# Optimization experiments

Measured on AMD Instinct MI355X. Metric: run time of the kernel, lower is better.

## Reference

```python
import jax, jax.numpy as jnp
import numpy as np

B, L, CIN, C = 256, 65, 2053, 512
SCALE = 1.0 / float(np.sqrt(C))


def _attn_layer(x, Wq, bq, Wk, bk, Wv, bv):
    # x: [B, Cin, L]; Conv1d(kernel=1) == channel-mixing matmul
    q = jnp.einsum('oi,bil->bol', Wq, x) + bq[:, None]
    k = jnp.einsum('oi,bil->bol', Wk, x) + bk[:, None]
    v = jax.nn.leaky_relu(jnp.einsum('oi,bil->bol', Wv, x) + bv[:, None], 0.01)
    # att[b,l,m] = <q[:,l], k[:,m]> / sqrt(C); softmax over m
    att = jax.nn.softmax(jnp.einsum('bcl,bcm->blm', q, k) * SCALE, axis=-1)
    # original: sum_m att[b,l,1,m] * v[b,1,c,m] -> [B,L,C] -> permute -> [B,C,L]
    out = jnp.einsum('blm,bcm->bcl', att, v)
    return out + x if out.shape == x.shape else out  # residual only when channels match


def _transform(x, Wq0, bq0, Wk0, bk0, Wv0, bv0, Wq, bq, Wk, bk, Wv, bv):
    x = _attn_layer(x, Wq0, bq0, Wk0, bk0, Wv0, bv0)
    for n in range(3):  # layers 1..3, C->C with residual
        x = _attn_layer(x, Wq[n], bq[n], Wk[n], bk[n], Wv[n], bv[n])
    return x


def setup_inputs():
    key = jax.random.key(0)
    ks = jax.random.split(key, 20)
    s = 0.02
    inp = {
        'dataleft': jax.random.normal(ks[0], (B, L, CIN), jnp.float32),
        'dataright': jax.random.normal(ks[1], (B, L, CIN), jnp.float32),
        # layer-0 QKV conv1d (k=1) weights: [C, CIN]
        'Wq0': jax.random.normal(ks[2], (C, CIN), jnp.float32) * s,
        'bq0': jnp.zeros((C,), jnp.float32),
        'Wk0': jax.random.normal(ks[3], (C, CIN), jnp.float32) * s,
        'bk0': jnp.zeros((C,), jnp.float32),
        'Wv0': jax.random.normal(ks[4], (C, CIN), jnp.float32) * s,
        'bv0': jnp.zeros((C,), jnp.float32),
        # layers 1..3 stacked: [3, C, C]
        'Wq': jax.random.normal(ks[5], (3, C, C), jnp.float32) * s,
        'bq': jnp.zeros((3, C), jnp.float32),
        'Wk': jax.random.normal(ks[6], (3, C, C), jnp.float32) * s,
        'bk': jnp.zeros((3, C), jnp.float32),
        'Wv': jax.random.normal(ks[7], (3, C, C), jnp.float32) * s,
        'bv': jnp.zeros((3, C), jnp.float32),
        # classifier: fc1(1024->256), fc2(256->2)
        'W1': jax.random.normal(ks[8], (256, 2 * C), jnp.float32) * s,
        'b1': jnp.zeros((256,), jnp.float32),
        'W2': jax.random.normal(ks[9], (2, 256), jnp.float32) * s,
        'b2': jnp.zeros((2,), jnp.float32),
    }
    return inp


def reference(dataleft, dataright, Wq0, bq0, Wk0, bk0, Wv0, bv0,
              Wq, bq, Wk, bk, Wv, bv, W1, b1, W2, b2):
    xl = jnp.transpose(dataleft, (0, 2, 1))   # [B, CIN, L]
    xr = jnp.transpose(dataright, (0, 2, 1))
    xl = _transform(xl, Wq0, bq0, Wk0, bk0, Wv0, bv0, Wq, bq, Wk, bk, Wv, bv)
    xr = _transform(xr, Wq0, bq0, Wk0, bk0, Wv0, bv0, Wq, bq, Wk, bk, Wv, bv)
    # AdaptiveAvgPool2d((512,1)) on [B,512,L]: identity over channel dim, mean over L
    xl = jnp.mean(xl, axis=-1)  # [B, C]
    xr = jnp.mean(xr, axis=-1)
    h = jnp.concatenate([xl, xr], axis=1)            # [B, 2C]
    h = jax.nn.relu(h @ W1.T + b1)                   # [B, 256]
    y = h @ W2.T + b2                                # [B, 2]
    return y  # training mode: no final softmax
```

## Files before the change

### kernel.cpp

```cpp
#include <hip/hip_runtime.h>
#include <hip/hip_bf16.h>

#define BF16 __hip_bfloat16

typedef __bf16 bf16x8 __attribute__((ext_vector_type(8)));
typedef float f32x4 __attribute__((ext_vector_type(4)));

__device__ __forceinline__ void async_copy16(const void* g, void* l) {
    __builtin_amdgcn_global_load_lds(
        (const __attribute__((address_space(1))) void*)g,
        (__attribute__((address_space(3))) void*)l,
        16, 0, 0);
}

__global__ __launch_bounds__(256) void convert_pad_k(
    const float* __restrict__ src, BF16* __restrict__ dst,
    int Ks, int Kd) {
    const long r = blockIdx.y;
    const int k = (blockIdx.x * 256 + threadIdx.x) * 4;
    if (k >= Kd) return;
    const float* s = src + r * (long)Ks;
    float a0 = (k < Ks) ? s[k] : 0.f;
    float a1 = (k + 1 < Ks) ? s[k + 1] : 0.f;
    float a2 = (k + 2 < Ks) ? s[k + 2] : 0.f;
    float a3 = (k + 3 < Ks) ? s[k + 3] : 0.f;
    BF16 b0 = __float2bfloat16(a0), b1 = __float2bfloat16(a1);
    BF16 b2 = __float2bfloat16(a2), b3 = __float2bfloat16(a3);
    ushort4 o = make_ushort4(*(ushort*)&b0, *(ushort*)&b1, *(ushort*)&b2, *(ushort*)&b3);
    *(ushort4*)&dst[r * (long)Kd + k] = o;
}

template <int K>
__device__ __forceinline__ void gemm_body(
    const BF16* __restrict__ Xg, const BF16* __restrict__ Wg,
    const float* __restrict__ bqp, const float* __restrict__ bkp, const float* __restrict__ bvp,
    BF16* __restrict__ Qo, BF16* __restrict__ Ko, BF16* __restrict__ Vo) {
    __shared__ __align__(16) BF16 As[3][256 * 32];
    __shared__ __align__(16) BF16 Bs[3][128 * 32];
    const int tid = threadIdx.x;
    const int w = tid >> 6;
    const int lane = tid & 63;
    const int quad = lane >> 4;
    const int l15 = lane & 15;
    const int linear = blockIdx.x + 12 * blockIdx.y;
    const int cpx = (12 * (int)gridDim.y) >> 3;
    const int id2 = (linear & 7) * cpx + (linear >> 3);
    const int bx = id2 % 12;
    const int by = id2 / 12;
    const long n0 = (long)by * 256;
    const long m0full = (long)bx * 128;
    const int sel = bx >> 2;
    const int mbase = (bx & 3) * 128;
    const int wr = (w >> 1) * 64;
    const int wc = (w & 1) * 64;
    constexpr int KT = K >> 5;
    const int rw = w * 16 + (lane >> 2);
    const int gsw = ((lane & 3) ^ ((lane >> 3) & 3)) * 8;
    const int gx = (quad ^ ((l15 >> 1) & 3)) * 8;

#define STAGE_TILE(k0, buf)                                                              \
    do {                                                                                 \
        _Pragma("unroll")                                                                \
        for (int r_ = 0; r_ < 2; ++r_)                                                   \
            async_copy16(Xg + (n0 + r_ * 128 + rw) * K + (k0) + gsw,                     \
                         &As[buf][(r_ * 128 + w * 16) * 32]);                            \
        async_copy16(Wg + (m0full + rw) * K + (k0) + gsw,                                \
                     &Bs[buf][(w * 16) * 32]);                                           \
    } while (0)

    f32x4 acc[4][4] = {};
    STAGE_TILE(0, 0);
    STAGE_TILE(32, 1);
    int cb = 0;
    for (int kt = 0; kt < KT; ++kt) {
        if (kt + 1 < KT) {
            asm volatile("s_waitcnt vmcnt(3)\n\ts_barrier" ::: "memory");
        } else {
            asm volatile("s_waitcnt vmcnt(0)\n\ts_barrier" ::: "memory");
        }
        __builtin_amdgcn_sched_barrier(0);
        bf16x8 af[4], bfr[4];
#pragma unroll
        for (int i = 0; i < 4; ++i)
            af[i] = *(const bf16x8*)&As[cb][(wr + i * 16 + l15) * 32 + gx];
#pragma unroll
        for (int j = 0; j < 4; ++j)
            bfr[j] = *(const bf16x8*)&Bs[cb][(wc + j * 16 + l15) * 32 + gx];
        if (kt + 2 < KT) {
            int nb = cb + 2;
            if (nb >= 3) nb -= 3;
            STAGE_TILE((kt + 2) << 5, nb);
        }
        __builtin_amdgcn_s_setprio(1);
#pragma unroll
        for (int i = 0; i < 4; ++i)
#pragma unroll
            for (int j = 0; j < 4; ++j)
                acc[i][j] = __builtin_amdgcn_mfma_f32_16x16x32_bf16(af[i], bfr[j], acc[i][j], 0, 0, 0);
        __builtin_amdgcn_s_setprio(0);
        ++cb;
        if (cb >= 3) cb -= 3;
    }
#undef STAGE_TILE

    const float* bp = (sel == 0) ? bqp : (sel == 1) ? bkp : bvp;
    BF16* out = (sel == 0) ? Qo : (sel == 1) ? Ko : Vo;
#pragma unroll
    for (int j = 0; j < 4; ++j) {
        const int m = mbase + wc + j * 16 + l15;
        const float bz = bp[m];
#pragma unroll
        for (int i = 0; i < 4; ++i) {
#pragma unroll
            for (int r = 0; r < 4; ++r) {
                const long n = n0 + wr + i * 16 + quad * 4 + r;
                float v = acc[i][j][r] + bz;
                if (sel == 2) v = (v >= 0.f) ? v : 0.01f * v;
                out[n * 512 + m] = __float2bfloat16(v);
            }
        }
    }
}

__global__ __launch_bounds__(512, 2) void gemm_k2112(
    const BF16* __restrict__ Xg, const BF16* __restrict__ Wg,
    const float* __restrict__ bqp, const float* __restrict__ bkp, const float* __restrict__ bvp,
    BF16* __restrict__ Qo, BF16* __restrict__ Ko, BF16* __restrict__ Vo) {
    gemm_body<2112>(Xg, Wg, bqp, bkp, bvp, Qo, Ko, Vo);
}

__global__ __launch_bounds__(512, 2) void gemm_k512(
    const BF16* __restrict__ Xg, const BF16* __restrict__ Wg,
    const float* __restrict__ bqp, const float* __restrict__ bkp, const float* __restrict__ bvp,
    BF16* __restrict__ Qo, BF16* __restrict__ Ko, BF16* __restrict__ Vo) {
    gemm_body<512>(Xg, Wg, bqp, bkp, bvp, Qo, Ko, Vo);
}

__global__ __launch_bounds__(256) void attn_fused(
    const BF16* __restrict__ Qg, const BF16* __restrict__ Kg, const BF16* __restrict__ Vg,
    BF16* __restrict__ Xg, int residual) {
    constexpr float SC = 0.04419417382415922f;
    __shared__ __align__(16) char Us[26624];
    __shared__ float Sf[80 * 84];
    __shared__ __align__(16) BF16 Pl[80 * 104];
    BF16* qk = (BF16*)Us;
    BF16* Vtl = (BF16*)Us;
    const int bb = blockIdx.x;
    const int tid = threadIdx.x;
    const int w = tid >> 6, lane = tid & 63, quad = lane >> 4, l15 = lane & 15;

    int i16a[7], j16a[7];
#pragma unroll
    for (int u = 0; u < 7; ++u) {
        const int t = w + 4 * u;
        const int tc = (t < 25) ? t : 0;
        i16a[u] = (tc / 5) * 16;
        j16a[u] = (tc % 5) * 16;
    }
    f32x4 acc[7] = {};
    for (int k0 = 0; k0 < 512; k0 += 64) {
        for (int idx = tid; idx < 1280; idx += 256) {
            const int t = (idx >= 640) ? 1 : 0;
            const int e = idx - t * 640;
            const int sub = (e >= 320) ? 1 : 0;
            const int e2 = e - sub * 320;
            const int row = e2 >> 2;
            const int koff = (e2 & 3) * 8;
            uint4 val = make_uint4(0, 0, 0, 0);
            if (row < 65) {
                const BF16* src = (t ? Kg : Qg) + ((long)(bb * 65 + row) * 512 + k0 + sub * 32 + koff);
                val = *(const uint4*)src;
            }
            *(uint4*)&qk[(t * 2 + sub) * 2560 + row * 32 + koff] = val;
        }
        __syncthreads();
#pragma unroll
        for (int sub = 0; sub < 2; ++sub) {
#pragma unroll
            for (int u = 0; u < 7; ++u) {
                if (w + 4 * u < 25) {
                    bf16x8 af = *(const bf16x8*)&qk[sub * 2560 + (i16a[u] + l15) * 32 + quad * 8];
                    bf16x8 bfr = *(const bf16x8*)&qk[(2 + sub) * 2560 + (j16a[u] + l15) * 32 + quad * 8];
                    acc[u] = __builtin_amdgcn_mfma_f32_16x16x32_bf16(af, bfr, acc[u], 0, 0, 0);
                }
            }
        }
        __syncthreads();
    }
#pragma unroll
    for (int u = 0; u < 7; ++u) {
        if (w + 4 * u < 25) {
#pragma unroll
            for (int r = 0; r < 4; ++r)
                Sf[(i16a[u] + quad * 4 + r) * 84 + j16a[u] + l15] = acc[u][r] * SC;
        }
    }
    __syncthreads();
    for (int rr = tid >> 2; rr < 65; rr += 64) {
        const int sub = tid & 3;
        float mx = -1e30f;
        for (int m = sub; m < 65; m += 4) mx = fmaxf(mx, Sf[rr * 84 + m]);
        mx = fmaxf(mx, __shfl_xor(mx, 1));
        mx = fmaxf(mx, __shfl_xor(mx, 2));
        float s = 0.f;
        for (int m = sub; m < 65; m += 4) {
            float e = __expf(Sf[rr * 84 + m] - mx);
            Sf[rr * 84 + m] = e;
            s += e;
        }
        s += __shfl_xor(s, 1);
        s += __shfl_xor(s, 2);
        const float inv = 1.f / s;
        for (int m = sub; m < 96; m += 4) {
            float v = (m < 65) ? Sf[rr * 84 + m] * inv : 0.f;
            Pl[rr * 104 + m] = __float2bfloat16(v);
        }
    }
    for (int idx = tid; idx < 15 * 48; idx += 256) {
        const int row = 65 + idx / 48;
        const int col = (idx - (idx / 48) * 48) * 2;
        *(uint*)&Pl[row * 104 + col] = 0u;
    }
    for (int idx = tid; idx < 128 * 32; idx += 256) {
        const int m = 65 + (idx & 31);
        if (m < 96) Vtl[(idx >> 5) * 104 + m] = (BF16)0.f;
    }
    __syncthreads();

    bf16x8 af[5][3];
#pragma unroll
    for (int i = 0; i < 5; ++i)
#pragma unroll
        for (int ks = 0; ks < 3; ++ks)
            af[i][ks] = *(const bf16x8*)&Pl[(i * 16 + l15) * 104 + ks * 32 + quad * 8];

    for (int cc = 0; cc < 4; ++cc) {
        const int c0 = cc * 128;
        for (int idx = tid; idx < 65 * 16; idx += 256) {
            const int m = idx >> 4;
            const int cg = idx & 15;
            uint4 val = *(const uint4*)(Vg + ((long)(bb * 65 + m) * 512 + c0 + cg * 8));
            const ushort* u = (const ushort*)&val;
#pragma unroll
            for (int j = 0; j < 8; ++j)
                *(ushort*)&Vtl[(cg * 8 + j) * 104 + m] = u[j];
        }
        __syncthreads();
#pragma unroll
        for (int jj = 0; jj < 2; ++jj) {
            const int ch = (jj * 4 + w) * 16 + l15;
            const int c = c0 + ch;
            bf16x8 b0 = *(const bf16x8*)&Vtl[ch * 104 + quad * 8];
            bf16x8 b1 = *(const bf16x8*)&Vtl[ch * 104 + 32 + quad * 8];
            bf16x8 b2 = *(const bf16x8*)&Vtl[ch * 104 + 64 + quad * 8];
            f32x4 po[5] = {};
#pragma unroll
            for (int i = 0; i < 5; ++i) {
                po[i] = __builtin_amdgcn_mfma_f32_16x16x32_bf16(af[i][0], b0, po[i], 0, 0, 0);
                po[i] = __builtin_amdgcn_mfma_f32_16x16x32_bf16(af[i][1], b1, po[i], 0, 0, 0);
                po[i] = __builtin_amdgcn_mfma_f32_16x16x32_bf16(af[i][2], b2, po[i], 0, 0, 0);
            }
#pragma unroll
            for (int i = 0; i < 5; ++i)
#pragma unroll
                for (int r = 0; r < 4; ++r) {
                    const int l = i * 16 + quad * 4 + r;
                    if (l < 65) {
                        const long idx = ((long)(bb * 65 + l)) * 512 + c;
                        float v = po[i][r];
                        if (residual) v += __bfloat162float(Xg[idx]);
                        Xg[idx] = __float2bfloat16(v);
                    }
                }
        }
        __syncthreads();
    }
}

__global__ __launch_bounds__(256) void pool_k(const BF16* __restrict__ Xg,
                                              float* __restrict__ Hp) {
    const int sb = blockIdx.x;
    const int s = sb >> 8, b = sb & 255;
    for (int c = threadIdx.x; c < 512; c += 256) {
        float acc = 0.f;
        for (int l = 0; l < 65; ++l)
            acc += __bfloat162float(Xg[((long)sb * 65 + l) * 512 + c]);
        Hp[(long)b * 1024 + s * 512 + c] = acc * (1.f / 65.f);
    }
}

__global__ __launch_bounds__(256) void fc_k(
    const float* __restrict__ Hp, const float* __restrict__ W1,
    const float* __restrict__ b1, const float* __restrict__ W2,
    const float* __restrict__ b2, float* __restrict__ out) {
    __shared__ float h[1024];
    __shared__ float h1[256];
    const int b = blockIdx.x, tid = threadIdx.x;
    for (int k = tid; k < 1024; k += 256) h[k] = Hp[(long)b * 1024 + k];
    __syncthreads();
    float acc = b1[tid];
    for (int k = 0; k < 1024; ++k) acc += W1[(long)tid * 1024 + k] * h[k];
    h1[tid] = fmaxf(acc, 0.f);
    __syncthreads();
    const int w = tid >> 6, lane = tid & 63;
    if (w < 2) {
        float p = 0.f;
        for (int u = lane; u < 256; u += 64) p += W2[w * 256 + u] * h1[u];
        for (int off = 32; off > 0; off >>= 1) p += __shfl_down(p, off);
        if (lane == 0) out[b * 2 + w] = p + b2[w];
    }
}

extern "C" void kernel_launch(void* const* d_in, const int* in_sizes, int n_in,
                              void* d_out, int out_size, void* d_ws, size_t ws_size,
                              hipStream_t stream) {
    const float* dataL = (const float*)d_in[0];
    const float* dataR = (const float*)d_in[1];
    const float* Wq0 = (const float*)d_in[2];
    const float* bq0 = (const float*)d_in[3];
    const float* Wk0 = (const float*)d_in[4];
    const float* bk0 = (const float*)d_in[5];
    const float* Wv0 = (const float*)d_in[6];
    const float* bv0 = (const float*)d_in[7];
    const float* Wq = (const float*)d_in[8];
    const float* bq = (const float*)d_in[9];
    const float* Wk = (const float*)d_in[10];
    const float* bk = (const float*)d_in[11];
    const float* Wv = (const float*)d_in[12];
    const float* bv = (const float*)d_in[13];
    const float* W1 = (const float*)d_in[14];
    const float* b1 = (const float*)d_in[15];
    const float* W2 = (const float*)d_in[16];
    const float* b2 = (const float*)d_in[17];

    char* ws = (char*)d_ws;
    BF16* Xb = (BF16*)ws;
    BF16* X = Xb;
    float* Hp = (float*)(ws + 90800128L);
    BF16* Wc = (BF16*)(ws + 140574720L);
    BF16* Qb = (BF16*)(ws + 151781376L);
    BF16* Kb = (BF16*)(ws + 185860096L);
    BF16* Vb = (BF16*)(ws + 219938816L);

    BF16* w0 = Wc;
    BF16* wl = Wc + 3L * 512 * 2112;

    auto cvt = [&](const float* src, BF16* dst, long R, int Ks, int Kd) {
        dim3 grid((Kd / 4 + 255) / 256, (unsigned)R);
        convert_pad_k<<<grid, 256, 0, stream>>>(src, dst, Ks, Kd);
    };
    cvt(dataL, Xb, 16640, 2053, 2112);
    cvt(dataR, Xb + 16640L * 2112, 16640, 2053, 2112);
    cvt(Wq0, w0, 512, 2053, 2112);
    cvt(Wk0, w0 + 512L * 2112, 512, 2053, 2112);
    cvt(Wv0, w0 + 2L * 512 * 2112, 512, 2053, 2112);
    for (int n = 0; n < 3; ++n) {
        BF16* base = wl + (long)n * 3 * 262144;
        cvt(Wq + (long)n * 262144, base, 512, 512, 512);
        cvt(Wk + (long)n * 262144, base + 262144, 512, 512, 512);
        cvt(Wv + (long)n * 262144, base + 2 * 262144, 512, 512, 512);
    }

    dim3 ggrid(12, 130);
    gemm_k2112<<<ggrid, 512, 0, stream>>>(Xb, w0, bq0, bk0, bv0, Qb, Kb, Vb);
    attn_fused<<<512, 256, 0, stream>>>(Qb, Kb, Vb, X, 0);
    for (int n = 0; n < 3; ++n) {
        gemm_k512<<<ggrid, 512, 0, stream>>>(X, wl + (long)n * 3 * 262144,
                                             bq + n * 512, bk + n * 512, bv + n * 512,
                                             Qb, Kb, Vb);
        attn_fused<<<512, 256, 0, stream>>>(Qb, Kb, Vb, X, 1);
    }
    pool_k<<<512, 256, 0, stream>>>(X, Hp);
    fc_k<<<256, 256, 0, stream>>>(Hp, W1, b1, W2, b2, (float*)d_out);
}
```

Before: 1.166 ms.

## Enlarge QKV GEMM tile to 256x256 with split A-fragment MFMA phases

The QKV projection GEMM block tile grows from 256x128 to 256x256, so each of the 8 waves computes a 128x64 sub-tile with 8x4 accumulators. The k-loop is split into two halves that load the low and high A fragments separately and interleave async global-to-LDS staging between them. Grid swizzling now handles non-multiple-of-8 workgroup counts across XCDs, and the layer-0 GEMM is launched as two half-grid kernels. The larger tile increases reuse per loaded byte and halves the number of blocks, at the cost of more LDS and accumulator registers, which may lower occupancy.

```diff
diff --git a/kernel.cpp b/kernel.cpp
--- a/kernel.cpp
+++ b/kernel.cpp
@@ -34,87 +34,103 @@
 __device__ __forceinline__ void gemm_body(
     const BF16* __restrict__ Xg, const BF16* __restrict__ Wg,
     const float* __restrict__ bqp, const float* __restrict__ bkp, const float* __restrict__ bvp,
-    BF16* __restrict__ Qo, BF16* __restrict__ Ko, BF16* __restrict__ Vo) {
+    BF16* __restrict__ Qo, BF16* __restrict__ Ko, BF16* __restrict__ Vo, int nbase) {
     __shared__ __align__(16) BF16 As[3][256 * 32];
-    __shared__ __align__(16) BF16 Bs[3][128 * 32];
+    __shared__ __align__(16) BF16 Bs[3][256 * 32];
     const int tid = threadIdx.x;
-    const int w = tid >> 6;
-    const int lane = tid & 63;
-    const int quad = lane >> 4;
-    const int l15 = lane & 15;
-    const int linear = blockIdx.x + 12 * blockIdx.y;
-    const int cpx = (12 * (int)gridDim.y) >> 3;
-    const int id2 = (linear & 7) * cpx + (linear >> 3);
-    const int bx = id2 % 12;
-    const int by = id2 / 12;
-    const long n0 = (long)by * 256;
-    const long m0full = (long)bx * 128;
-    const int sel = bx >> 2;
-    const int mbase = (bx & 3) * 128;
-    const int wr = (w >> 1) * 64;
-    const int wc = (w & 1) * 64;
+    const int w = tid >> 6, lane = tid & 63, quad = lane >> 4, l15 = lane & 15;
+    const int wn2 = (w >> 2) * 128;
+    const int wm4 = (w & 3) * 64;
+    const int nwg = 6 * (int)gridDim.y;
+    const int orig = blockIdx.x + 6 * blockIdx.y;
+    const int qq = nwg >> 3, rr = nwg & 7;
+    const int xcd = orig & 7, loc = orig >> 3;
+    const int id2 = (xcd < rr ? xcd * (qq + 1) : rr * (qq + 1) + (xcd - rr) * qq) + loc;
+    const int bx = id2 % 6;
+    const int by = id2 / 6;
+    const long n0 = ((long)nbase + by) * 256;
+    const long m0 = (long)bx * 256;
+    const int sel = bx >> 1;
+    const int mb = (bx & 1) * 256;
     constexpr int KT = K >> 5;
-    const int rw = w * 16 + (lane >> 2);
-    const int gsw = ((lane & 3) ^ ((lane >> 3) & 3)) * 8;
-    const int gx = (quad ^ ((l15 >> 1) & 3)) * 8;
-
-#define STAGE_TILE(k0, buf)                                                              \
-    do {                                                                                 \
-        _Pragma("unroll")                                                                \
-        for (int r_ = 0; r_ < 2; ++r_)                                                   \
-            async_copy16(Xg + (n0 + r_ * 128 + rw) * K + (k0) + gsw,                     \
-                         &As[buf][(r_ * 128 + w * 16) * 32]);                            \
-        async_copy16(Wg + (m0full + rw) * K + (k0) + gsw,                                \
-                     &Bs[buf][(w * 16) * 32]);                                           \
-    } while (0)
-
-    f32x4 acc[4][4] = {};
-    STAGE_TILE(0, 0);
-    STAGE_TILE(32, 1);
+    const int srow = tid >> 2;
+    const int gsw = ((tid & 3) ^ (srow & 3)) * 8;
+    const int gx = (quad ^ (l15 & 3)) * 8;
+
+    f32x4 acc[8][4] = {};
+#pragma unroll
+    for (int t = 0; t < 2; ++t) {
+        async_copy16(Xg + (n0 + srow) * K + t * 32 + gsw, &As[t][w * 512]);
+        async_copy16(Xg + (n0 + 128 + srow) * K + t * 32 + gsw, &As[t][4096 + w * 512]);
+        async_copy16(Wg + (m0 + srow) * K + t * 32 + gsw, &Bs[t][w * 512]);
+        async_copy16(Wg + (m0 + 128 + srow) * K + t * 32 + gsw, &Bs[t][4096 + w * 512]);
+    }
     int cb = 0;
     for (int kt = 0; kt < KT; ++kt) {
         if (kt + 1 < KT) {
-            asm volatile("s_waitcnt vmcnt(3)\n\ts_barrier" ::: "memory");
+            asm volatile("s_waitcnt vmcnt(4)\n\ts_barrier" ::: "memory");
         } else {
             asm volatile("s_waitcnt vmcnt(0)\n\ts_barrier" ::: "memory");
         }
         __builtin_amdgcn_sched_barrier(0);
-        bf16x8 af[4], bfr[4];
-#pragma unroll
-        for (int i = 0; i < 4; ++i)
-            af[i] = *(const bf16x8*)&As[cb][(wr + i * 16 + l15) * 32 + gx];
+        const BF16* Ab = &As[cb][0];
+        const BF16* Bb = &Bs[cb][0];
+        int ns = cb + 2;
+        if (ns >= 3) ns -= 3;
+        const long kn = (long)(kt + 2) << 5;
+        bf16x8 bfr[4], afl[4];
 #pragma unroll
         for (int j = 0; j < 4; ++j)
-            bfr[j] = *(const bf16x8*)&Bs[cb][(wc + j * 16 + l15) * 32 + gx];
+            bfr[j] = *(const bf16x8*)&Bb[(wm4 + j * 16 + l15) * 32 + gx];
+#pragma unroll
+        for (int f = 0; f < 4; ++f)
+            afl[f] = *(const bf16x8*)&Ab[(wn2 + f * 16 + l15) * 32 + gx];
         if (kt + 2 < KT) {
-            int nb = cb + 2;
-            if (nb >= 3) nb -= 3;
-            STAGE_TILE((kt + 2) << 5, nb);
-        }
+            async_copy16(Xg + (n0 + srow) * K + kn + gsw, &As[ns][w * 512]);
+            async_copy16(Wg + (m0 + srow) * K + kn + gsw, &Bs[ns][w * 512]);
+        }
+        asm volatile("s_waitcnt lgkmcnt(0)" ::: "memory");
+        __builtin_amdgcn_sched_barrier(0);
         __builtin_amdgcn_s_setprio(1);
 #pragma unroll
-        for (int i = 0; i < 4; ++i)
+        for (int f = 0; f < 4; ++f)
 #pragma unroll
             for (int j = 0; j < 4; ++j)
-                acc[i][j] = __builtin_amdgcn_mfma_f32_16x16x32_bf16(af[i], bfr[j], acc[i][j], 0, 0, 0);
+                acc[f][j] = __builtin_amdgcn_mfma_f32_16x16x32_bf16(afl[f], bfr[j], acc[f][j], 0, 0, 0);
+        __builtin_amdgcn_s_setprio(0);
+        bf16x8 afh[4];
+#pragma unroll
+        for (int f = 0; f < 4; ++f)
+            afh[f] = *(const bf16x8*)&Ab[(wn2 + 64 + f * 16 + l15) * 32 + gx];
+        if (kt + 2 < KT) {
+            async_copy16(Xg + (n0 + 128 + srow) * K + kn + gsw, &As[ns][4096 + w * 512]);
+            async_copy16(Wg + (m0 + 128 + srow) * K + kn + gsw, &Bs[ns][4096 + w * 512]);
+        }
+        asm volatile("s_waitcnt lgkmcnt(0)" ::: "memory");
+        __builtin_amdgcn_sched_barrier(0);
+        __builtin_amdgcn_s_setprio(1);
+#pragma unroll
+        for (int f = 0; f < 4; ++f)
+#pragma unroll
+            for (int j = 0; j < 4; ++j)
+                acc[f + 4][j] = __builtin_amdgcn_mfma_f32_16x16x32_bf16(afh[f], bfr[j], acc[f + 4][j], 0, 0, 0);
         __builtin_amdgcn_s_setprio(0);
         ++cb;
         if (cb >= 3) cb -= 3;
     }
-#undef STAGE_TILE
 
     const float* bp = (sel == 0) ? bqp : (sel == 1) ? bkp : bvp;
     BF16* out = (sel == 0) ? Qo : (sel == 1) ? Ko : Vo;
 #pragma unroll
     for (int j = 0; j < 4; ++j) {
-        const int m = mbase + wc + j * 16 + l15;
+        const int m = mb + wm4 + j * 16 + l15;
         const float bz = bp[m];
 #pragma unroll
-        for (int i = 0; i < 4; ++i) {
+        for (int f = 0; f < 8; ++f) {
 #pragma unroll
             for (int r = 0; r < 4; ++r) {
-                const long n = n0 + wr + i * 16 + quad * 4 + r;
-                float v = acc[i][j][r] + bz;
+                const long n = n0 + wn2 + f * 16 + quad * 4 + r;
+                float v = acc[f][j][r] + bz;
                 if (sel == 2) v = (v >= 0.f) ? v : 0.01f * v;
                 out[n * 512 + m] = __float2bfloat16(v);
             }
@@ -122,18 +138,25 @@
     }
 }
 
-__global__ __launch_bounds__(512, 2) void gemm_k2112(
+__global__ __launch_bounds__(512, 2) void gemm_k2112_lo(
     const BF16* __restrict__ Xg, const BF16* __restrict__ Wg,
     const float* __restrict__ bqp, const float* __restrict__ bkp, const float* __restrict__ bvp,
     BF16* __restrict__ Qo, BF16* __restrict__ Ko, BF16* __restrict__ Vo) {
-    gemm_body<2112>(Xg, Wg, bqp, bkp, bvp, Qo, Ko, Vo);
+    gemm_body<2112>(Xg, Wg, bqp, bkp, bvp, Qo, Ko, Vo, 0);
+}
+
+__global__ __launch_bounds__(512, 2) void gemm_k2112_hi(
+    const BF16* __restrict__ Xg, const BF16* __restrict__ Wg,
+    const float* __restrict__ bqp, const float* __restrict__ bkp, const float* __restrict__ bvp,
+    BF16* __restrict__ Qo, BF16* __restrict__ Ko, BF16* __restrict__ Vo) {
+    gemm_body<2112>(Xg, Wg, bqp, bkp, bvp, Qo, Ko, Vo, 65);
 }
 
 __global__ __launch_bounds__(512, 2) void gemm_k512(
     const BF16* __restrict__ Xg, const BF16* __restrict__ Wg,
     const float* __restrict__ bqp, const float* __restrict__ bkp, const float* __restrict__ bvp,
     BF16* __restrict__ Qo, BF16* __restrict__ Ko, BF16* __restrict__ Vo) {
-    gemm_body<512>(Xg, Wg, bqp, bkp, bvp, Qo, Ko, Vo);
+    gemm_body<512>(Xg, Wg, bqp, bkp, bvp, Qo, Ko, Vo, 0);
 }
 
 __global__ __launch_bounds__(256) void attn_fused(
@@ -361,11 +384,13 @@
         cvt(Wv + (long)n * 262144, base + 2 * 262144, 512, 512, 512);
     }
 
-    dim3 ggrid(12, 130);
-    gemm_k2112<<<ggrid, 512, 0, stream>>>(Xb, w0, bq0, bk0, bv0, Qb, Kb, Vb);
+    dim3 ghalf(6, 65);
+    dim3 gfull(6, 130);
+    gemm_k2112_lo<<<ghalf, 512, 0, stream>>>(Xb, w0, bq0, bk0, bv0, Qb, Kb, Vb);
+    gemm_k2112_hi<<<ghalf, 512, 0, stream>>>(Xb, w0, bq0, bk0, bv0, Qb, Kb, Vb);
     attn_fused<<<512, 256, 0, stream>>>(Qb, Kb, Vb, X, 0);
     for (int n = 0; n < 3; ++n) {
-        gemm_k512<<<ggrid, 512, 0, stream>>>(X, wl + (long)n * 3 * 262144,
+        gemm_k512<<<gfull, 512, 0, stream>>>(X, wl + (long)n * 3 * 262144,
                                              bq + n * 512, bk + n * 512, bv + n * 512,
                                              Qb, Kb, Vb);
         attn_fused<<<512, 256, 0, stream>>>(Qb, Kb, Vb, X, 1);
```

After: 1.309 ms. 12.3% more time.
